# Kernel optimization log

Hardware: AMD Instinct MI355X
Metric: run time of the kernel (lower is better)

Reference implementation:

```python
import jax, jax.numpy as jnp
import numpy as np
import math

N_CELLS = 65536
HIDDEN = 128
IN_DIM = 64
MAX_DEG = 6
BOND_P = 0.5


def _build_graph():
    """2D lattice bond percolation -> padded adjacency [n, MAX_DEG] + signs + mask."""
    rng = np.random.default_rng(0)
    side = int(math.ceil(math.sqrt(N_CELLS)))
    adj = [[] for _ in range(N_CELLS)]
    for i in range(N_CELLS):
        col = i % side
        r = i + 1
        if col + 1 < side and r < N_CELLS and rng.random() < BOND_P:
            adj[i].append(r); adj[r].append(i)
        d = i + side
        if d < N_CELLS and rng.random() < BOND_P:
            adj[i].append(d); adj[d].append(i)
    for i in range(N_CELLS):  # ring fix for isolated nodes
        if not adj[i]:
            r = (i + 1) % N_CELLS
            adj[i].append(r); adj[r].append(i)
    sign_map = {}
    for i in range(N_CELLS):
        for j in adj[i]:
            key = (min(i, j), max(i, j))
            if key not in sign_map:
                sign_map[key] = 1.0 if rng.random() > 0.5 else -1.0
    nbr = np.zeros((N_CELLS, MAX_DEG), np.int32)
    sgn = np.ones((N_CELLS, MAX_DEG), np.float32)
    msk = np.zeros((N_CELLS, MAX_DEG), bool)
    for i in range(N_CELLS):
        for k, j in enumerate(adj[i][:MAX_DEG]):
            nbr[i, k] = j
            msk[i, k] = True
            sgn[i, k] = sign_map[(min(i, j), max(i, j))]
    return nbr, sgn, msk


def setup_inputs() -> dict:
    key = jax.random.key(0)
    ks = jax.random.split(key, 8)
    nbr, sgn, msk = _build_graph()
    n = N_CELLS
    cell_amp = jax.random.uniform(ks[0], (n, HIDDEN)) * 0.5 + 0.5
    cell_phase = jax.random.normal(ks[1], (n, HIDDEN)) * 0.5 \
        + (2.0 * jnp.pi * jnp.arange(n, dtype=jnp.float32) / n)[:, None]
    phase_vel = jax.random.normal(ks[2], (n, HIDDEN)) * 0.05
    return {
        'x': jax.random.normal(ks[3], (1, IN_DIM)),
        'cell_amp': cell_amp.astype(jnp.float32),
        'cell_phase': cell_phase.astype(jnp.float32),
        'phase_vel': phase_vel.astype(jnp.float32),
        'nbr_idx': jnp.asarray(nbr),
        'nbr_sign': jnp.asarray(sgn),
        'nbr_mask': jnp.asarray(msk),
        'W_in': jax.random.normal(ks[4], (HIDDEN, IN_DIM)) * 0.05,
        'b_in': jax.random.normal(ks[5], (HIDDEN,)) * 0.05,
        'W_dec': jax.random.normal(ks[6], (IN_DIM, 2 * HIDDEN)) * 0.05,
        'b_dec': jax.random.normal(ks[7], (IN_DIM,)) * 0.05,
        'step': 1,
    }


def reference(x, cell_amp, cell_phase, phase_vel, nbr_idx, nbr_sign, nbr_mask,
              W_in, b_in, W_dec, b_dec, step):
    n, h = cell_amp.shape
    # complex cell states, then phase-velocity rotation
    states = (cell_amp * jnp.exp(1j * cell_phase)).astype(jnp.complex64)
    states = states * jnp.exp(1j * phase_vel * 0.1)
    ang = jnp.angle(states)                               # [n, h]

    # --- neighbor interference (vectorized gather over padded adjacency) ---
    nbr_states = states[nbr_idx]                          # [n, d, h]
    nbr_ang = ang[nbr_idx]                                # [n, d, h]
    coupling = jnp.cos(ang[:, None, :] - nbr_ang) * nbr_sign[:, :, None]
    contrib = jnp.where(nbr_mask[:, :, None], coupling * nbr_states * 0.1, 0.0)
    interference = contrib.sum(axis=1)                    # [n, h]
    deg = nbr_mask.sum(axis=-1)                           # [n]
    new = 0.7 * states + 0.3 * interference / jnp.maximum(deg, 1)[:, None]
    new = jnp.where((deg > 0)[:, None], new, states)      # 'continue' for isolated nodes

    # --- morphism toward strongest neighbor (argmax over neighbors) ---
    strength = jnp.abs(states).sum(axis=-1)               # [n]
    nstr = jnp.where(nbr_mask, strength[nbr_idx], -jnp.inf)
    best_slot = jnp.argmax(nstr, axis=1)                  # first max, like python max()
    best = jnp.take_along_axis(nbr_idx, best_slot[:, None], axis=1)[:, 0]
    src = states[best]                                    # [n, h]
    morph = jnp.abs(src) * jnp.exp(1j * (jnp.angle(new) - jnp.angle(src)))
    new = jnp.where((deg >= 2)[:, None], new + 0.02 * morph, new)

    # --- global traveling wave ---
    t = step * 0.1
    wave = 0.02 * jnp.sin(t + 2.0 * jnp.pi * jnp.arange(n, dtype=jnp.float32) / n)
    new = new * (1.0 + wave)[:, None]

    # --- input-driven phase perturbation on first 32 cells ---
    sig = x[0] @ W_in.T + b_in                            # [h]
    pp = sig / (jnp.abs(sig).max() + 1e-8) * jnp.pi * 0.1
    idx = jnp.arange(n, dtype=jnp.float32)
    factor = jnp.where(jnp.arange(n) < 32, 0.1 / (1.0 + 0.1 * idx), 0.0)
    new_ang = jnp.angle(new) + pp[None, :] * factor[:, None]
    new = jnp.abs(new) * jnp.exp(1j * new_ang)

    # --- amplitude renormalization per cell ---
    amp = jnp.abs(new)
    amp = amp / (amp.max(axis=-1, keepdims=True) + 1e-8)
    cs = (amp * jnp.exp(1j * jnp.angle(new))).astype(jnp.complex64)

    # --- readout ---
    mean_state = cs.mean(axis=0)                          # [h]
    out_real = jnp.concatenate([mean_state.real, mean_state.imag])[None, :]
    pred = out_real @ W_dec.T + b_dec                     # [1, IN_DIM]
    tension = jnp.var(jnp.abs(cs), ddof=1)                # torch.var (unbiased)
    return pred, tension
```

## Files before the change

kernel.cpp:

```cpp
#include <hip/hip_runtime.h>
#include <hip/hip_fp16.h>
#include <math.h>

#define N_CELLS 65536
#define HIDDEN  128
#define IN_DIM  64
#define MAX_DEG 6

#define WPB    4
#define NPB    32
#define NBLK   (N_CELLS/NPB)
#define CHUNK  4

#define INV2PI 0.15915494309189535f

__device__ __forceinline__ void fsincos(float x, float& s, float& c) {
    const float r = x * INV2PI;
    s = __builtin_amdgcn_sinf(r);
    c = __builtin_amdgcn_cosf(r);
}

#define WS_PP    0
#define WS_FLAG  512
#define WS_STR   1024
#define WS_S     (1024 + N_CELLS*4)
#define WS_P     (WS_S + (size_t)N_CELLS*512)
#define WS_SA    (WS_P + 256*NBLK*4)
#define WS_SA2   (WS_SA + NBLK*4)
#define WS_MEAN  (WS_SA2 + NBLK*4)

__global__ __launch_bounds__(256) void k_pre(
    const float* __restrict__ amp, const float* __restrict__ phase,
    const float* __restrict__ vel,
    const float* __restrict__ x, const float* __restrict__ W_in,
    const float* __restrict__ b_in, const unsigned char* __restrict__ maskb,
    int4* __restrict__ S, float* __restrict__ strength,
    float* __restrict__ pp, int* __restrict__ flag)
{
    const int tid = threadIdx.x;
    if (blockIdx.x < N_CELLS/8) {
        const int node = blockIdx.x*8 + (tid >> 5);
        const int hl   = tid & 31;
        const size_t ro = (size_t)node*HIDDEN + 4*hl;
        const float4 a = *(const float4*)(amp   + ro);
        const float4 p = *(const float4*)(phase + ro);
        const float4 v = *(const float4*)(vel   + ro);
        float s0,c0,s1,c1,s2,c2,s3,c3;
        fsincos(fmaf(0.1f, v.x, p.x), s0, c0);
        fsincos(fmaf(0.1f, v.y, p.y), s1, c1);
        fsincos(fmaf(0.1f, v.z, p.z), s2, c2);
        fsincos(fmaf(0.1f, v.w, p.w), s3, c3);
        union { int4 v4; __half2 h[4]; } u;
        u.h[0] = __floats2half2_rn(a.x*c0, a.x*s0);
        u.h[1] = __floats2half2_rn(a.y*c1, a.y*s1);
        u.h[2] = __floats2half2_rn(a.z*c2, a.z*s2);
        u.h[3] = __floats2half2_rn(a.w*c3, a.w*s3);
        S[(size_t)node*32 + hl] = u.v4;
        float st = a.x + a.y + a.z + a.w;
        #pragma unroll
        for (int off = 16; off > 0; off >>= 1) st += __shfl_xor(st, off);
        if (hl == 0) strength[node] = st;
        return;
    }
    __shared__ float sig[HIDDEN];
    __shared__ float red[HIDDEN];
    __shared__ int fl[256];
    if (tid < HIDDEN) {
        float acc = b_in[tid];
        #pragma unroll 8
        for (int d = 0; d < IN_DIM; ++d) acc = fmaf(W_in[tid*IN_DIM + d], x[d], acc);
        sig[tid] = acc;
        red[tid] = fabsf(acc);
    }
    int v = 0;
    #pragma unroll
    for (int r = 0; r < 4; ++r) v |= (int)maskb[(tid + 256*r)*4 + 1];
    fl[tid] = v;
    __syncthreads();
    for (int s = 64; s > 0; s >>= 1) {
        if (tid < s) red[tid] = fmaxf(red[tid], red[tid + s]);
        __syncthreads();
    }
    for (int s = 128; s > 0; s >>= 1) {
        if (tid < s) fl[tid] |= fl[tid + s];
        __syncthreads();
    }
    if (tid < HIDDEN) pp[tid] = sig[tid] / (red[0] + 1e-8f) * 0.314159265358979f;
    if (tid == 0) *flag = (fl[0] != 0) ? 1 : 0;
}

__global__ __launch_bounds__(256) void k_mainc(
    const int4* __restrict__ S, const int* __restrict__ nbr_idx,
    const float* __restrict__ nbr_sign, const void* __restrict__ nbr_mask,
    const int* __restrict__ step, const float* __restrict__ pp,
    const int* __restrict__ flagp, const float* __restrict__ strength,
    float* __restrict__ P, float* __restrict__ p_sa, float* __restrict__ p_sa2)
{
    __shared__ int   lji[NPB][MAX_DEG];
    __shared__ float lsk[NPB][MAX_DEG];
    __shared__ int   lwp[NPB][8];
    __shared__ float4 lredre[WPB][32], lredim[WPB][32];
    __shared__ float  lsa[WPB], lsa2[WPB];

    const int tid   = threadIdx.x;
    const int blk   = blockIdx.x;
    const int node0 = blk * NPB;

    if (tid < NPB*MAX_DEG) {
        const int flagv = *flagp;
        const unsigned char* mb = (const unsigned char*)nbr_mask;
        const int*           mi = (const int*)nbr_mask;
        const int n = tid / MAX_DEG, k = tid - n*MAX_DEG;
        const int e = (node0 + n)*MAX_DEG + k;
        const int m = flagv ? (mb[e] != 0) : (mi[e] != 0);
        const int j = nbr_idx[e];
        const float sg = nbr_sign[e];
        lji[n][k] = m ? (j | ((sg < 0.0f) ? (1<<24) : 0) | (1<<25)) : 0;
        lsk[n][k] = m ? strength[j] : -3.0e38f;
    }
    __syncthreads();
    if (tid < NPB) {
        int cnt = 0, jb = 0; float bv = -3.0e38f;
        #pragma unroll
        for (int k = 0; k < MAX_DEG; ++k) {
            const int w = lji[tid][k];
            if (w >> 25) lwp[tid][cnt++] = w;
            const float sv = lsk[tid][k];
            if (sv > bv) { bv = sv; jb = w & 0xFFFF; }
        }
        for (int k = cnt; k < MAX_DEG; ++k) lwp[tid][k] = 0;
        lwp[tid][6] = cnt;
        lwp[tid][7] = jb;
    }
    __syncthreads();

    const int wv   = tid >> 6;
    const int lane = tid & 63;
    const int half = lane >> 5;
    const int lh   = lane & 31;
    const float trev = 0.1f * (float)step[0] * INV2PI;
    const float4 ppv = ((const float4*)pp)[lh];

    float accre[4] = {0,0,0,0}, accim[4] = {0,0,0,0};
    float accsa = 0.f, accsa2 = 0.f;

    #pragma unroll 1
    for (int c = 0; c < CHUNK; ++c) {
        const int nl = wv*(2*CHUNK) + 2*c + half;
        const int i  = node0 + nl;
        const int4 A0 = *(const int4*)&lwp[nl][0];
        const int4 A1 = *(const int4*)&lwp[nl][4];
        const int deg = A1.z, jb = A1.w;
        const int kmax = max(deg, __shfl_xor(deg, 32));

        const int slots[MAX_DEG] = {A0.x, A0.y, A0.z, A0.w, A1.x, A1.y};

        union H { int4 v4; __half2 h[4]; };
        H us, ub, nb[MAX_DEG];
        us.v4 = S[(size_t)(unsigned)i *32 + lh];
        ub.v4 = S[(size_t)(unsigned)jb*32 + lh];
        #pragma unroll
        for (int k = 0; k < MAX_DEG; ++k)
            if (k < kmax) nb[k].v4 = S[(size_t)(unsigned)(slots[k] & 0xFFFF)*32 + lh];

        float R[4], I[4], inva[4];
        #pragma unroll
        for (int q = 0; q < 4; ++q) {
            const float2 e = __half22float2(us.h[q]);
            R[q] = e.x; I[q] = e.y;
            inva[q] = __builtin_amdgcn_rsqf(e.x*e.x + e.y*e.y);
        }

        float ir[4] = {0,0,0,0}, ii[4] = {0,0,0,0};
        #pragma unroll
        for (int k = 0; k < MAX_DEG; ++k) {
            if (k < kmax) {
                const int w = slots[k];
                const float sgnm = (w & (1<<25)) ? ((w & (1<<24)) ? -1.0f : 1.0f) : 0.0f;
                #pragma unroll
                for (int q = 0; q < 4; ++q) {
                    const float2 e = __half22float2(nb[k].h[q]);
                    const float E = R[q]*e.x + I[q]*e.y;
                    const float g = sgnm * E * __builtin_amdgcn_rsqf(e.x*e.x + e.y*e.y);
                    ir[q] = fmaf(g, e.x, ir[q]);
                    ii[q] = fmaf(g, e.y, ii[q]);
                }
            }
        }

        const float f = 0.03f * __builtin_amdgcn_rcpf((float)deg);
        float nr[4], ni[4];
        #pragma unroll
        for (int q = 0; q < 4; ++q) {
            const float fq = f * inva[q];
            nr[q] = fmaf(0.7f, R[q], fq*ir[q]);
            ni[q] = fmaf(0.7f, I[q], fq*ii[q]);
        }

        if (deg >= 2) {
            #pragma unroll
            for (int q = 0; q < 4; ++q) {
                const float2 e = __half22float2(ub.h[q]);
                const float im = 0.02f * __builtin_amdgcn_rsqf(nr[q]*nr[q] + ni[q]*ni[q]);
                const float mr = im*(nr[q]*e.x + ni[q]*e.y);
                const float mi = im*(ni[q]*e.x - nr[q]*e.y);
                nr[q] += mr; ni[q] += mi;
            }
        }

        const float wr = fmaf((float)i, 1.52587890625e-5f, trev);
        const float wf = 1.0f + 0.02f * __builtin_amdgcn_sinf(wr);
        #pragma unroll
        for (int q = 0; q < 4; ++q) { nr[q] *= wf; ni[q] *= wf; }

        if (i < 32) {
            const float fac = 0.1f / fmaf(0.1f, (float)i, 1.0f);
            const float pv[4] = {ppv.x, ppv.y, ppv.z, ppv.w};
            #pragma unroll
            for (int q = 0; q < 4; ++q) {
                float sp, cp;
                fsincos(pv[q]*fac, sp, cp);
                const float tr = nr[q]*cp - ni[q]*sp;
                ni[q] = ni[q]*cp + nr[q]*sp;
                nr[q] = tr;
            }
        }

        float m[4];
        #pragma unroll
        for (int q = 0; q < 4; ++q) m[q] = sqrtf(nr[q]*nr[q] + ni[q]*ni[q]);
        float lm = fmaxf(fmaxf(m[0], m[1]), fmaxf(m[2], m[3]));
        #pragma unroll
        for (int off = 16; off > 0; off >>= 1) lm = fmaxf(lm, __shfl_xor(lm, off));
        const float sc = 1.0f / (lm + 1e-8f);
        #pragma unroll
        for (int q = 0; q < 4; ++q) {
            accre[q] += nr[q]*sc;
            accim[q] += ni[q]*sc;
            const float A = m[q]*sc;
            accsa  += A;
            accsa2 += A*A;
        }
    }

    #pragma unroll
    for (int q = 0; q < 4; ++q) {
        accre[q] += __shfl_xor(accre[q], 32);
        accim[q] += __shfl_xor(accim[q], 32);
    }
    #pragma unroll
    for (int off = 32; off > 0; off >>= 1) {
        accsa  += __shfl_xor(accsa,  off);
        accsa2 += __shfl_xor(accsa2, off);
    }
    if (half == 0) {
        lredre[wv][lh] = make_float4(accre[0], accre[1], accre[2], accre[3]);
        lredim[wv][lh] = make_float4(accim[0], accim[1], accim[2], accim[3]);
    }
    if (lane == 0) { lsa[wv] = accsa; lsa2[wv] = accsa2; }
    __syncthreads();
    if (tid < 32) {
        float4 r = lredre[0][tid], im = lredim[0][tid];
        #pragma unroll
        for (int w = 1; w < WPB; ++w) {
            const float4 a = lredre[w][tid], b = lredim[w][tid];
            r.x += a.x; r.y += a.y; r.z += a.z; r.w += a.w;
            im.x += b.x; im.y += b.y; im.z += b.z; im.w += b.w;
        }
        P[(4*tid  )*NBLK + blk]       = r.x;
        P[(4*tid+1)*NBLK + blk]       = r.y;
        P[(4*tid+2)*NBLK + blk]       = r.z;
        P[(4*tid+3)*NBLK + blk]       = r.w;
        P[(128+4*tid  )*NBLK + blk]   = im.x;
        P[(128+4*tid+1)*NBLK + blk]   = im.y;
        P[(128+4*tid+2)*NBLK + blk]   = im.z;
        P[(128+4*tid+3)*NBLK + blk]   = im.w;
    }
    if (tid == 0) {
        p_sa [blk] = lsa[0]  + lsa[1]  + lsa[2]  + lsa[3];
        p_sa2[blk] = lsa2[0] + lsa2[1] + lsa2[2] + lsa2[3];
    }
}

__global__ void k_red(const float* __restrict__ P, float* __restrict__ mean)
{
    __shared__ double red[256];
    const int r = blockIdx.x, tid = threadIdx.x;
    double s = 0.0;
    #pragma unroll
    for (int k = 0; k < NBLK/256; ++k) s += (double)P[(size_t)r*NBLK + tid + 256*k];
    red[tid] = s;
    __syncthreads();
    for (int st = 128; st > 0; st >>= 1) { if (tid < st) red[tid] += red[tid + st]; __syncthreads(); }
    if (tid == 0) mean[r] = (float)(red[0] / (double)N_CELLS);
}

__global__ void k_final(const float* __restrict__ mean_in,
                        const float* __restrict__ p_sa, const float* __restrict__ p_sa2,
                        const float* __restrict__ W_dec, const float* __restrict__ b_dec,
                        float* __restrict__ out)
{
    __shared__ float  mean[2*HIDDEN];
    __shared__ double dred[256];
    __shared__ double tots[2];
    const int tid = threadIdx.x;
    mean[tid] = mean_in[tid];
    double sa = 0.0, sa2 = 0.0;
    #pragma unroll
    for (int k = 0; k < NBLK/256; ++k) {
        sa  += (double)p_sa [tid + 256*k];
        sa2 += (double)p_sa2[tid + 256*k];
    }
    dred[tid] = sa;
    __syncthreads();
    for (int s = 128; s > 0; s >>= 1) { if (tid < s) dred[tid] += dred[tid + s]; __syncthreads(); }
    if (tid == 0) tots[0] = dred[0];
    __syncthreads();
    dred[tid] = sa2;
    __syncthreads();
    for (int s = 128; s > 0; s >>= 1) { if (tid < s) dred[tid] += dred[tid + s]; __syncthreads(); }
    if (tid == 0) tots[1] = dred[0];
    __syncthreads();

    if (tid < IN_DIM) {
        float acc = b_dec[tid];
        #pragma unroll 8
        for (int c = 0; c < 2*HIDDEN; ++c) acc = fmaf(mean[c], W_dec[tid*2*HIDDEN + c], acc);
        out[tid] = acc;
    }
    if (tid == 0) {
        const double M = (double)N_CELLS * (double)HIDDEN;
        const double var = (tots[1] - tots[0]*tots[0]/M) / (M - 1.0);
        out[IN_DIM] = (float)var;
    }
}

extern "C" void kernel_launch(void* const* d_in, const int* in_sizes, int n_in,
                              void* d_out, int out_size, void* d_ws, size_t ws_size,
                              hipStream_t stream)
{
    const float* x       = (const float*)d_in[0];
    const float* amp     = (const float*)d_in[1];
    const float* phase   = (const float*)d_in[2];
    const float* vel     = (const float*)d_in[3];
    const int*   nbr_idx = (const int*)d_in[4];
    const float* nbr_sgn = (const float*)d_in[5];
    const void*  nbr_msk = d_in[6];
    const float* W_in    = (const float*)d_in[7];
    const float* b_in    = (const float*)d_in[8];
    const float* W_dec   = (const float*)d_in[9];
    const float* b_dec   = (const float*)d_in[10];
    const int*   step    = (const int*)d_in[11];

    char* wsb = (char*)d_ws;
    float* pp    = (float*)(wsb + WS_PP);
    int*   flag  = (int*)  (wsb + WS_FLAG);
    float* strg  = (float*)(wsb + WS_STR);
    int4*  S     = (int4*) (wsb + WS_S);
    float* P     = (float*)(wsb + WS_P);
    float* p_sa  = (float*)(wsb + WS_SA);
    float* p_sa2 = (float*)(wsb + WS_SA2);
    float* meanb = (float*)(wsb + WS_MEAN);
    float* out   = (float*)d_out;

    k_pre<<<N_CELLS/8 + 1, 256, 0, stream>>>(amp, phase, vel, x, W_in, b_in,
                                             (const unsigned char*)nbr_msk,
                                             S, strg, pp, flag);
    k_mainc<<<NBLK, 256, 0, stream>>>(S, nbr_idx, nbr_sgn, nbr_msk,
                                      step, pp, flag, strg, P, p_sa, p_sa2);
    k_red<<<256, 256, 0, stream>>>(P, meanb);
    k_final<<<1, 256, 0, stream>>>(meanb, p_sa, p_sa2, W_dec, b_dec, out);
}
```

Baseline: 67.77 us.

## Reuse loaded neighbor rows for strongest neighbor and swizzle blocks across XCDs

The strongest neighbor's state row is now picked by register select from the already-loaded neighbor rows, so the extra global gather for it is gone. Block indices are remapped so contiguous node ranges land on the same XCD, aiming for better L2 locality on lattice neighbors. The per-pair max degree is precomputed in shared memory instead of using a cross-lane shuffle. These add an extra barrier and some select instructions per chunk.

Measured after the change: 67.78 us. About the same (+0.0%).

```diff
diff --git a/kernel.cpp b/kernel.cpp
--- a/kernel.cpp
+++ b/kernel.cpp
@@ -11,6 +11,7 @@
 #define NPB    32
 #define NBLK   (N_CELLS/NPB)
 #define CHUNK  4
+#define NXCD   8
 
 #define INV2PI 0.15915494309189535f
 
@@ -99,11 +100,13 @@
     __shared__ int   lji[NPB][MAX_DEG];
     __shared__ float lsk[NPB][MAX_DEG];
     __shared__ int   lwp[NPB][8];
+    __shared__ int   kmx[NPB/2];
     __shared__ float4 lredre[WPB][32], lredim[WPB][32];
     __shared__ float  lsa[WPB], lsa2[WPB];
 
     const int tid   = threadIdx.x;
-    const int blk   = blockIdx.x;
+    const int bx    = blockIdx.x;
+    const int blk   = (bx & (NXCD-1)) * (NBLK/NXCD) + (bx >> 3);
     const int node0 = blk * NPB;
 
     if (tid < NPB*MAX_DEG) {
@@ -120,18 +123,24 @@
     }
     __syncthreads();
     if (tid < NPB) {
-        int cnt = 0, jb = 0; float bv = -3.0e38f;
+        int cnt = 0;
         #pragma unroll
         for (int k = 0; k < MAX_DEG; ++k) {
             const int w = lji[tid][k];
-            if (w >> 25) lwp[tid][cnt++] = w;
             const float sv = lsk[tid][k];
-            if (sv > bv) { bv = sv; jb = w & 0xFFFF; }
-        }
-        for (int k = cnt; k < MAX_DEG; ++k) lwp[tid][k] = 0;
+            if (w >> 25) { lwp[tid][cnt] = w; lsk[tid][cnt] = sv; ++cnt; }
+        }
+        #pragma unroll
+        for (int k = 0; k < MAX_DEG; ++k) if (k >= cnt) lwp[tid][k] = 0;
+        int cb = 0; float bv = lsk[tid][0];
+        #pragma unroll
+        for (int k = 1; k < MAX_DEG; ++k)
+            if (k < cnt && lsk[tid][k] > bv) { bv = lsk[tid][k]; cb = k; }
         lwp[tid][6] = cnt;
-        lwp[tid][7] = jb;
-    }
+        lwp[tid][7] = cb;
+    }
+    __syncthreads();
+    if (tid < NPB/2) kmx[tid] = max(lwp[2*tid][6], lwp[2*tid+1][6]);
     __syncthreads();
 
     const int wv   = tid >> 6;
@@ -150,15 +159,14 @@
         const int i  = node0 + nl;
         const int4 A0 = *(const int4*)&lwp[nl][0];
         const int4 A1 = *(const int4*)&lwp[nl][4];
-        const int deg = A1.z, jb = A1.w;
-        const int kmax = max(deg, __shfl_xor(deg, 32));
+        const int deg = A1.z, cb = A1.w;
+        const int kmax = kmx[wv*CHUNK + c];
 
         const int slots[MAX_DEG] = {A0.x, A0.y, A0.z, A0.w, A1.x, A1.y};
 
-        union H { int4 v4; __half2 h[4]; };
-        H us, ub, nb[MAX_DEG];
-        us.v4 = S[(size_t)(unsigned)i *32 + lh];
-        ub.v4 = S[(size_t)(unsigned)jb*32 + lh];
+        union H { int4 v4; __half2 h[4]; int w[4]; };
+        H us, nb[MAX_DEG];
+        us.v4 = S[(size_t)(unsigned)i*32 + lh];
         #pragma unroll
         for (int k = 0; k < MAX_DEG; ++k)
             if (k < kmax) nb[k].v4 = S[(size_t)(unsigned)(slots[k] & 0xFFFF)*32 + lh];
@@ -188,6 +196,16 @@
             }
         }
 
+        H ub;
+        #pragma unroll
+        for (int q = 0; q < 4; ++q) {
+            int v = nb[0].w[q];
+            #pragma unroll
+            for (int k = 1; k < MAX_DEG; ++k)
+                if (k < kmax) v = (k == cb) ? nb[k].w[q] : v;
+            ub.w[q] = v;
+        }
+
         const float f = 0.03f * __builtin_amdgcn_rcpf((float)deg);
         float nr[4], ni[4];
         #pragma unroll
```
